# Optimization experiments

Measured on AMD Instinct MI355X. Metric: run time of the kernel, lower is better.

The kernel has to match this reference:

```python
import jax, jax.numpy as jnp
import numpy as np

N_NODES = 100000

def setup_inputs() -> dict:
    key = jax.random.key(0)
    k1, k2, k3, k4 = jax.random.split(key, 4)
    nfeat, nhid = 128, 128
    features = jax.random.normal(k1, (N_NODES, nfeat), dtype=jnp.float32)
    edges = jax.random.randint(k2, (2, 1600000), 0, N_NODES, dtype=jnp.int64)
    # Linear(nfeature, nhidden) params (PyTorch layout: W [out, in], b [out])
    bound = 1.0 / np.sqrt(nfeat)
    W = jax.random.uniform(k3, (nhid, nfeat), dtype=jnp.float32, minval=-bound, maxval=bound)
    b = jax.random.uniform(k4, (nhid,), dtype=jnp.float32, minval=-bound, maxval=bound)
    return {"features": features, "edges": edges, "W": W, "b": b}

def reference(features, edges, W, b):
    n = features.shape[0]
    # add self loops
    loops = jnp.arange(n, dtype=edges.dtype)
    row = jnp.concatenate([edges[0], loops])  # source
    col = jnp.concatenate([edges[1], loops])  # target
    # linear transform
    x = features @ W.T + b  # [N, nhid]
    # degree over source indices (PyG message uses degree(row, size[0]))
    deg = jax.ops.segment_sum(jnp.ones_like(row, dtype=x.dtype), row, num_segments=n)
    dis = jax.lax.rsqrt(deg)  # deg >= 1 thanks to self loops
    norm = dis[row] * dis[col]  # [E']
    msgs = norm[:, None] * x[row]  # gather + scale, [E', nhid]
    out = jax.ops.segment_sum(msgs, col, num_segments=n)  # scatter-add to targets
    return out
```

## Files before the change

kernel.cpp:

```cpp
#include <hip/hip_runtime.h>

#define NFEAT 128
#define CH 25600
#define CH2 (CH / 2)

typedef __attribute__((ext_vector_type(8))) short bf16x8;
typedef __attribute__((ext_vector_type(4))) float f32x4;

static __device__ __forceinline__ short f2bf(float f) {
    unsigned u = __builtin_bit_cast(unsigned, f);
    unsigned r = (u + 0x7fff + ((u >> 16) & 1)) >> 16;
    return (short)r;
}
static __device__ __forceinline__ float bf2f(short s) {
    unsigned u = ((unsigned)(unsigned short)s) << 16;
    return __builtin_bit_cast(float, u);
}

__launch_bounds__(256)
__global__ void hist16_kernel(const int* __restrict__ rows, const int* __restrict__ cols,
                              unsigned int* __restrict__ ph_row, unsigned int* __restrict__ ph_col,
                              int* __restrict__ rank, int E, int n, int W, int log_epb) {
    __shared__ unsigned int h[CH2];
    const int b = blockIdx.x;
    const int c0 = blockIdx.y * CH;
    const int z = blockIdx.z;
    const int* __restrict__ keys = z ? cols : rows;
    unsigned int* __restrict__ ph = z ? ph_col : ph_row;

    for (int i = threadIdx.x; i < CH2; i += 256) h[i] = 0;
    __syncthreads();

    const int lo = b << log_epb;
    const int hi = min(E, lo + (1 << log_epb));
    const int t = threadIdx.x;

    int full = (hi - lo) >> 10;
    for (int it = 0; it < full; ++it) {
        int e0 = lo + (it << 10) + t * 4;
        int4 kk = *(const int4*)(keys + e0);
        int k0 = kk.x - c0, k1 = kk.y - c0, k2 = kk.z - c0, k3 = kk.w - c0;
        if ((unsigned)k0 < CH) {
            unsigned old = atomicAdd(&h[k0 >> 1], 1u << ((k0 & 1) * 16));
            if (z) rank[e0 + 0] = (old >> ((k0 & 1) * 16)) & 0xffff;
        }
        if ((unsigned)k1 < CH) {
            unsigned old = atomicAdd(&h[k1 >> 1], 1u << ((k1 & 1) * 16));
            if (z) rank[e0 + 1] = (old >> ((k1 & 1) * 16)) & 0xffff;
        }
        if ((unsigned)k2 < CH) {
            unsigned old = atomicAdd(&h[k2 >> 1], 1u << ((k2 & 1) * 16));
            if (z) rank[e0 + 2] = (old >> ((k2 & 1) * 16)) & 0xffff;
        }
        if ((unsigned)k3 < CH) {
            unsigned old = atomicAdd(&h[k3 >> 1], 1u << ((k3 & 1) * 16));
            if (z) rank[e0 + 3] = (old >> ((k3 & 1) * 16)) & 0xffff;
        }
    }
    for (int e = lo + (full << 10) + t; e < hi; e += 256) {
        int k = keys[e] - c0;
        if ((unsigned)k < CH) {
            unsigned old = atomicAdd(&h[k >> 1], 1u << ((k & 1) * 16));
            if (z) rank[e] = (old >> ((k & 1) * 16)) & 0xffff;
        }
    }
    __syncthreads();

    int wbase = c0 >> 1;
    for (int i = threadIdx.x; i < CH2; i += 256) {
        int w = wbase + i;
        if (w < W) ph[(size_t)b * W + w] = h[i];
    }
}

__global__ void cum_kernel(const unsigned short* __restrict__ ph_row,
                           unsigned short* __restrict__ ph_col,
                           float* __restrict__ dis, int* __restrict__ colcnt, int NB, int n) {
    int k = blockIdx.x * 256 + threadIdx.x;
    if (k >= n) return;
    int rs = 0;
    for (int b = 0; b < NB; ++b) rs += ph_row[(size_t)b * n + k];
    dis[k] = rsqrtf(1.0f + (float)rs);
    int acc = 0;
    for (int b = 0; b < NB; ++b) {
        int v = ph_col[(size_t)b * n + k];
        ph_col[(size_t)b * n + k] = (unsigned short)acc;
        acc += v;
    }
    colcnt[k] = acc;
}

__global__ void scan_bsum_kernel(const int* __restrict__ cnt, int* __restrict__ bsum, int n) {
    __shared__ int s[256];
    int base = blockIdx.x * 1024;
    int t = threadIdx.x;
    int v = 0;
#pragma unroll
    for (int i = 0; i < 4; ++i) {
        int idx = base + t * 4 + i;
        if (idx < n) v += cnt[idx];
    }
    s[t] = v;
    __syncthreads();
    for (int o = 128; o > 0; o >>= 1) {
        if (t < o) s[t] += s[t + o];
        __syncthreads();
    }
    if (t == 0) bsum[blockIdx.x] = s[0];
}

__global__ void scan_top_kernel(int* __restrict__ bsum, int nb) {
    __shared__ int s[256];
    int t = threadIdx.x;
    int v = (t < nb) ? bsum[t] : 0;
    s[t] = v;
    __syncthreads();
    for (int o = 1; o < 256; o <<= 1) {
        int add = (t >= o) ? s[t - o] : 0;
        __syncthreads();
        s[t] += add;
        __syncthreads();
    }
    if (t < nb) bsum[t] = s[t] - v;
}

__global__ void scan_write_kernel(const int* __restrict__ cnt, const int* __restrict__ bsum,
                                  int* __restrict__ off, int n) {
    __shared__ int s[256];
    int base = blockIdx.x * 1024;
    int t = threadIdx.x;
    int v[4];
    int sum = 0;
#pragma unroll
    for (int i = 0; i < 4; ++i) {
        int idx = base + t * 4 + i;
        v[i] = (idx < n) ? cnt[idx] : 0;
        sum += v[i];
    }
    s[t] = sum;
    __syncthreads();
    for (int o = 1; o < 256; o <<= 1) {
        int add = (t >= o) ? s[t - o] : 0;
        __syncthreads();
        s[t] += add;
        __syncthreads();
    }
    int p = bsum[blockIdx.x] + s[t] - sum;
#pragma unroll
    for (int i = 0; i < 4; ++i) {
        int idx = base + t * 4 + i;
        if (idx < n) { off[idx] = p; p += v[i]; }
    }
}

__global__ void scatter2_kernel(const int* __restrict__ rows, const int* __restrict__ cols,
                                const int* __restrict__ rank, const unsigned short* __restrict__ ph_col,
                                const int* __restrict__ off, int* __restrict__ rows_buf,
                                int E, int n, int log_epb) {
    int base = blockIdx.x * 1024 + threadIdx.x;
#pragma unroll
    for (int u = 0; u < 4; ++u) {
        int e = base + u * 256;
        if (e < E) {
            int k = cols[e];
            int b = e >> log_epb;
            int pos = off[k] + (int)ph_col[(size_t)b * n + k] + rank[e];
            rows_buf[pos] = rows[e];
        }
    }
}

__launch_bounds__(256, 2)
__global__ void gemm_mfma_kernel(const float* __restrict__ feat, const float* __restrict__ W,
                                 const float* __restrict__ b, float* __restrict__ x, int n) {
    __shared__ short whi[16384];
    __shared__ short wlo[16384];

    const int t = threadIdx.x;

    {
        int c = t >> 1;
        int kbase = (t & 1) * 64;
        int ct = c >> 4;
        int cl = c & 15;
#pragma unroll
        for (int kc = 0; kc < 8; ++kc) {
            int k0 = kbase + kc * 8;
            const float4* src = (const float4*)(W + (size_t)c * NFEAT + k0);
            float4 fa = src[0];
            float4 fb = src[1];
            float fv[8] = {fa.x, fa.y, fa.z, fa.w, fb.x, fb.y, fb.z, fb.w};
            short h8[8], l8[8];
#pragma unroll
            for (int i = 0; i < 8; ++i) {
                short hi = f2bf(fv[i]);
                h8[i] = hi;
                l8[i] = f2bf(fv[i] - bf2f(hi));
            }
            int kq = k0 >> 5;
            int lane = ((k0 & 31) >> 3) * 16 + cl;
            int idx = ((ct * 4 + kq) * 64 + lane) * 8;
            *(bf16x8*)&whi[idx] = *(bf16x8*)h8;
            *(bf16x8*)&wlo[idx] = *(bf16x8*)l8;
        }
    }
    __syncthreads();

    const int lane = t & 63;
    const int w = t >> 6;
    const int r0 = blockIdx.x * 64 + w * 16;
    const int arow = r0 + (lane & 15);
    const int koff = (lane >> 4) * 8;

    bf16x8 ahi[4], alo[4];
#pragma unroll
    for (int kq = 0; kq < 4; ++kq) {
        float fv[8] = {0, 0, 0, 0, 0, 0, 0, 0};
        if (arow < n) {
            const float4* src = (const float4*)(feat + (size_t)arow * NFEAT + kq * 32 + koff);
            float4 fa = src[0];
            float4 fb = src[1];
            fv[0] = fa.x; fv[1] = fa.y; fv[2] = fa.z; fv[3] = fa.w;
            fv[4] = fb.x; fv[5] = fb.y; fv[6] = fb.z; fv[7] = fb.w;
        }
        short h8[8], l8[8];
#pragma unroll
        for (int i = 0; i < 8; ++i) {
            short hi = f2bf(fv[i]);
            h8[i] = hi;
            l8[i] = f2bf(fv[i] - bf2f(hi));
        }
        ahi[kq] = *(bf16x8*)h8;
        alo[kq] = *(bf16x8*)l8;
    }

#pragma unroll
    for (int ct = 0; ct < 8; ++ct) {
        f32x4 acc = {0.f, 0.f, 0.f, 0.f};
#pragma unroll
        for (int kq = 0; kq < 4; ++kq) {
            int idx = ((ct * 4 + kq) * 64 + lane) * 8;
            bf16x8 bh = *(const bf16x8*)&whi[idx];
            bf16x8 bl = *(const bf16x8*)&wlo[idx];
            acc = __builtin_amdgcn_mfma_f32_16x16x32_bf16(ahi[kq], bh, acc, 0, 0, 0);
            acc = __builtin_amdgcn_mfma_f32_16x16x32_bf16(alo[kq], bh, acc, 0, 0, 0);
            acc = __builtin_amdgcn_mfma_f32_16x16x32_bf16(ahi[kq], bl, acc, 0, 0, 0);
        }
        int col = ct * 16 + (lane & 15);
        float bb = b[col];
#pragma unroll
        for (int reg = 0; reg < 4; ++reg) {
            int row = r0 + (lane >> 4) * 4 + reg;
            if (row < n) x[(size_t)row * NFEAT + col] = acc[reg] + bb;
        }
    }
}

__launch_bounds__(256)
__global__ void gather_kernel(const int* __restrict__ rows_buf, const int* __restrict__ off,
                              const int* __restrict__ cnt, const float* __restrict__ x,
                              const float* __restrict__ dis, float* __restrict__ out, int n) {
    int lane = threadIdx.x & 63;
    int h = lane >> 5;
    int fl = lane & 31;
    int c = blockIdx.x * 4 + (threadIdx.x >> 6);
    if (c >= n) return;

    float disc = dis[c];
    int start = off[c];
    int len = cnt[c];
    const float4* x4 = (const float4*)x;

    float4 acc = make_float4(0.f, 0.f, 0.f, 0.f);
    if (h == 0) {
        float4 xv = x4[(size_t)c * 32 + fl];
        float sl = disc * disc;
        acc.x = xv.x * sl; acc.y = xv.y * sl; acc.z = xv.z * sl; acc.w = xv.w * sl;
    }

    for (int base = 0; base < len; base += 64) {
        int m = min(64, len - base);
        int r_l = 0;
        float nrm_l = 0.0f;
        if (lane < m) {
            r_l = rows_buf[start + base + lane];
            nrm_l = dis[r_l] * disc;
        }
        int pairs = (m + 1) >> 1;
#pragma unroll 4
        for (int jj = 0; jj < pairs; ++jj) {
            int src = 2 * jj + h;
            int r = __shfl(r_l, src);
            float nm = __shfl(nrm_l, src);
            float4 a = x4[(size_t)r * 32 + fl];
            acc.x = fmaf(a.x, nm, acc.x);
            acc.y = fmaf(a.y, nm, acc.y);
            acc.z = fmaf(a.z, nm, acc.z);
            acc.w = fmaf(a.w, nm, acc.w);
        }
    }

    acc.x += __shfl_xor(acc.x, 32);
    acc.y += __shfl_xor(acc.y, 32);
    acc.z += __shfl_xor(acc.z, 32);
    acc.w += __shfl_xor(acc.w, 32);

    if (h == 0) ((float4*)out)[(size_t)c * 32 + fl] = acc;
}

extern "C" void kernel_launch(void* const* d_in, const int* in_sizes, int n_in,
                              void* d_out, int out_size, void* d_ws, size_t ws_size,
                              hipStream_t stream) {
    const float* feat = (const float*)d_in[0];
    const int*   edges = (const int*)d_in[1];
    const float* W = (const float*)d_in[2];
    const float* b = (const float*)d_in[3];
    float* out = (float*)d_out;

    int n = in_sizes[0] / NFEAT;
    int E = in_sizes[1] / 2;
    const int* row = edges;
    const int* col = edges + E;

    int Wd = (n + 1) / 2;
    int nchunk = (n + CH - 1) / CH;

    size_t fixed = (size_t)n * NFEAT + 3 * (size_t)n + 2 * (size_t)E + 256;
    int log_epb = 16;
    int NB = (E + (1 << 16) - 1) >> 16;
    for (int lg = 14; lg <= 16; ++lg) {
        int nb_try = (E + (1 << lg) - 1) >> lg;
        size_t words = fixed + 2 * (size_t)nb_try * Wd;
        if (words * 4 <= ws_size) { log_epb = lg; NB = nb_try; break; }
    }

    float* x        = (float*)d_ws;
    float* dis      = x + (size_t)n * NFEAT;
    int*   colcnt   = (int*)(dis + n);
    int*   off      = colcnt + n;
    int*   rows_buf = off + n;
    int*   rank     = rows_buf + E;
    int*   bsum     = rank + E;
    unsigned int* ph_row = (unsigned int*)(bsum + 256);
    unsigned int* ph_col = ph_row + (size_t)NB * Wd;

    int nb = (n + 1023) / 1024;

    dim3 hgrid(NB, nchunk, 2);
    hist16_kernel<<<hgrid, 256, 0, stream>>>(row, col, ph_row, ph_col, rank, E, n, Wd, log_epb);

    cum_kernel<<<(n + 255) / 256, 256, 0, stream>>>((const unsigned short*)ph_row,
                                                    (unsigned short*)ph_col, dis, colcnt, NB, n);

    scan_bsum_kernel<<<nb, 256, 0, stream>>>(colcnt, bsum, n);
    scan_top_kernel<<<1, 256, 0, stream>>>(bsum, nb);
    scan_write_kernel<<<nb, 256, 0, stream>>>(colcnt, bsum, off, n);

    scatter2_kernel<<<(E + 1023) / 1024, 256, 0, stream>>>(row, col, rank,
                                                           (const unsigned short*)ph_col,
                                                           off, rows_buf, E, n, log_epb);

    gemm_mfma_kernel<<<(n + 63) / 64, 256, 0, stream>>>(feat, W, b, x, n);

    gather_kernel<<<(n + 3) / 4, 256, 0, stream>>>(rows_buf, off, colcnt, x, dis, out, n);
}
```

Measured before the change: 395.2 us.

## Store transformed features as bf16 and gather with quarter-wave rows

The GEMM drops the split-bf16 (hi/lo) three-MFMA emulation of fp32 and uses a single bf16 MFMA, then writes x as bf16 instead of fp32. This halves the intermediate buffer and the bytes moved in the gather. The gather kernel now lets each 16-lane quarter of a wave read one 256-byte bf16 row, so four edges are processed per step, and the partial sums are reduced across quarters with shuffles. Accuracy drops to plain bf16 for both the GEMM inputs and the stored activations, which may exceed the tolerance.

```diff
diff --git a/kernel.cpp b/kernel.cpp
--- a/kernel.cpp
+++ b/kernel.cpp
@@ -12,9 +12,11 @@
     unsigned r = (u + 0x7fff + ((u >> 16) & 1)) >> 16;
     return (short)r;
 }
-static __device__ __forceinline__ float bf2f(short s) {
-    unsigned u = ((unsigned)(unsigned short)s) << 16;
-    return __builtin_bit_cast(float, u);
+static __device__ __forceinline__ float bflo(unsigned u) {
+    return __builtin_bit_cast(float, u << 16);
+}
+static __device__ __forceinline__ float bfhi(unsigned u) {
+    return __builtin_bit_cast(float, u & 0xffff0000u);
 }
 
 __launch_bounds__(256)
@@ -170,11 +172,10 @@
     }
 }
 
-__launch_bounds__(256, 2)
-__global__ void gemm_mfma_kernel(const float* __restrict__ feat, const float* __restrict__ W,
-                                 const float* __restrict__ b, float* __restrict__ x, int n) {
-    __shared__ short whi[16384];
-    __shared__ short wlo[16384];
+__launch_bounds__(256)
+__global__ void gemm_bf16_kernel(const float* __restrict__ feat, const float* __restrict__ W,
+                                 const float* __restrict__ b, unsigned short* __restrict__ x16, int n) {
+    __shared__ short wb[16384];
 
     const int t = threadIdx.x;
 
@@ -190,18 +191,13 @@
             float4 fa = src[0];
             float4 fb = src[1];
             float fv[8] = {fa.x, fa.y, fa.z, fa.w, fb.x, fb.y, fb.z, fb.w};
-            short h8[8], l8[8];
-#pragma unroll
-            for (int i = 0; i < 8; ++i) {
-                short hi = f2bf(fv[i]);
-                h8[i] = hi;
-                l8[i] = f2bf(fv[i] - bf2f(hi));
-            }
+            short h8[8];
+#pragma unroll
+            for (int i = 0; i < 8; ++i) h8[i] = f2bf(fv[i]);
             int kq = k0 >> 5;
             int lane = ((k0 & 31) >> 3) * 16 + cl;
             int idx = ((ct * 4 + kq) * 64 + lane) * 8;
-            *(bf16x8*)&whi[idx] = *(bf16x8*)h8;
-            *(bf16x8*)&wlo[idx] = *(bf16x8*)l8;
+            *(bf16x8*)&wb[idx] = *(bf16x8*)h8;
         }
     }
     __syncthreads();
@@ -212,7 +208,7 @@
     const int arow = r0 + (lane & 15);
     const int koff = (lane >> 4) * 8;
 
-    bf16x8 ahi[4], alo[4];
+    bf16x8 a[4];
 #pragma unroll
     for (int kq = 0; kq < 4; ++kq) {
         float fv[8] = {0, 0, 0, 0, 0, 0, 0, 0};
@@ -223,15 +219,10 @@
             fv[0] = fa.x; fv[1] = fa.y; fv[2] = fa.z; fv[3] = fa.w;
             fv[4] = fb.x; fv[5] = fb.y; fv[6] = fb.z; fv[7] = fb.w;
         }
-        short h8[8], l8[8];
-#pragma unroll
-        for (int i = 0; i < 8; ++i) {
-            short hi = f2bf(fv[i]);
-            h8[i] = hi;
-            l8[i] = f2bf(fv[i] - bf2f(hi));
-        }
-        ahi[kq] = *(bf16x8*)h8;
-        alo[kq] = *(bf16x8*)l8;
+        short h8[8];
+#pragma unroll
+        for (int i = 0; i < 8; ++i) h8[i] = f2bf(fv[i]);
+        a[kq] = *(bf16x8*)h8;
     }
 
 #pragma unroll
@@ -240,43 +231,35 @@
 #pragma unroll
         for (int kq = 0; kq < 4; ++kq) {
             int idx = ((ct * 4 + kq) * 64 + lane) * 8;
-            bf16x8 bh = *(const bf16x8*)&whi[idx];
-            bf16x8 bl = *(const bf16x8*)&wlo[idx];
-            acc = __builtin_amdgcn_mfma_f32_16x16x32_bf16(ahi[kq], bh, acc, 0, 0, 0);
-            acc = __builtin_amdgcn_mfma_f32_16x16x32_bf16(alo[kq], bh, acc, 0, 0, 0);
-            acc = __builtin_amdgcn_mfma_f32_16x16x32_bf16(ahi[kq], bl, acc, 0, 0, 0);
+            bf16x8 bh = *(const bf16x8*)&wb[idx];
+            acc = __builtin_amdgcn_mfma_f32_16x16x32_bf16(a[kq], bh, acc, 0, 0, 0);
         }
         int col = ct * 16 + (lane & 15);
         float bb = b[col];
 #pragma unroll
         for (int reg = 0; reg < 4; ++reg) {
             int row = r0 + (lane >> 4) * 4 + reg;
-            if (row < n) x[(size_t)row * NFEAT + col] = acc[reg] + bb;
+            if (row < n) x16[(size_t)row * NFEAT + col] = (unsigned short)f2bf(acc[reg] + bb);
         }
     }
 }
 
 __launch_bounds__(256)
 __global__ void gather_kernel(const int* __restrict__ rows_buf, const int* __restrict__ off,
-                              const int* __restrict__ cnt, const float* __restrict__ x,
+                              const int* __restrict__ cnt, const unsigned short* __restrict__ x16,
                               const float* __restrict__ dis, float* __restrict__ out, int n) {
     int lane = threadIdx.x & 63;
-    int h = lane >> 5;
-    int fl = lane & 31;
+    int q = lane >> 4;
+    int fq = lane & 15;
     int c = blockIdx.x * 4 + (threadIdx.x >> 6);
     if (c >= n) return;
 
     float disc = dis[c];
     int start = off[c];
     int len = cnt[c];
-    const float4* x4 = (const float4*)x;
-
-    float4 acc = make_float4(0.f, 0.f, 0.f, 0.f);
-    if (h == 0) {
-        float4 xv = x4[(size_t)c * 32 + fl];
-        float sl = disc * disc;
-        acc.x = xv.x * sl; acc.y = xv.y * sl; acc.z = xv.z * sl; acc.w = xv.w * sl;
-    }
+    const uint4* xv = (const uint4*)x16;
+
+    float a0 = 0.f, a1 = 0.f, a2 = 0.f, a3 = 0.f, a4 = 0.f, a5 = 0.f, a6 = 0.f, a7 = 0.f;
 
     for (int base = 0; base < len; base += 64) {
         int m = min(64, len - base);
@@ -286,26 +269,42 @@
             r_l = rows_buf[start + base + lane];
             nrm_l = dis[r_l] * disc;
         }
-        int pairs = (m + 1) >> 1;
+        int quads = (m + 3) >> 2;
 #pragma unroll 4
-        for (int jj = 0; jj < pairs; ++jj) {
-            int src = 2 * jj + h;
+        for (int jj = 0; jj < quads; ++jj) {
+            int src = 4 * jj + q;
             int r = __shfl(r_l, src);
             float nm = __shfl(nrm_l, src);
-            float4 a = x4[(size_t)r * 32 + fl];
-            acc.x = fmaf(a.x, nm, acc.x);
-            acc.y = fmaf(a.y, nm, acc.y);
-            acc.z = fmaf(a.z, nm, acc.z);
-            acc.w = fmaf(a.w, nm, acc.w);
-        }
-    }
-
-    acc.x += __shfl_xor(acc.x, 32);
-    acc.y += __shfl_xor(acc.y, 32);
-    acc.z += __shfl_xor(acc.z, 32);
-    acc.w += __shfl_xor(acc.w, 32);
-
-    if (h == 0) ((float4*)out)[(size_t)c * 32 + fl] = acc;
+            if (src < m) {
+                uint4 v = xv[(size_t)r * 16 + fq];
+                a0 = fmaf(bflo(v.x), nm, a0); a1 = fmaf(bfhi(v.x), nm, a1);
+                a2 = fmaf(bflo(v.y), nm, a2); a3 = fmaf(bfhi(v.y), nm, a3);
+                a4 = fmaf(bflo(v.z), nm, a4); a5 = fmaf(bfhi(v.z), nm, a5);
+                a6 = fmaf(bflo(v.w), nm, a6); a7 = fmaf(bfhi(v.w), nm, a7);
+            }
+        }
+    }
+
+    a0 += __shfl_xor(a0, 16); a1 += __shfl_xor(a1, 16);
+    a2 += __shfl_xor(a2, 16); a3 += __shfl_xor(a3, 16);
+    a4 += __shfl_xor(a4, 16); a5 += __shfl_xor(a5, 16);
+    a6 += __shfl_xor(a6, 16); a7 += __shfl_xor(a7, 16);
+    a0 += __shfl_xor(a0, 32); a1 += __shfl_xor(a1, 32);
+    a2 += __shfl_xor(a2, 32); a3 += __shfl_xor(a3, 32);
+    a4 += __shfl_xor(a4, 32); a5 += __shfl_xor(a5, 32);
+    a6 += __shfl_xor(a6, 32); a7 += __shfl_xor(a7, 32);
+
+    if (q == 0) {
+        float sl = disc * disc;
+        uint4 v = xv[(size_t)c * 16 + fq];
+        a0 = fmaf(bflo(v.x), sl, a0); a1 = fmaf(bfhi(v.x), sl, a1);
+        a2 = fmaf(bflo(v.y), sl, a2); a3 = fmaf(bfhi(v.y), sl, a3);
+        a4 = fmaf(bflo(v.z), sl, a4); a5 = fmaf(bfhi(v.z), sl, a5);
+        a6 = fmaf(bflo(v.w), sl, a6); a7 = fmaf(bfhi(v.w), sl, a7);
+        float4* o = (float4*)(out + (size_t)c * NFEAT + fq * 8);
+        o[0] = make_float4(a0, a1, a2, a3);
+        o[1] = make_float4(a4, a5, a6, a7);
+    }
 }
 
 extern "C" void kernel_launch(void* const* d_in, const int* in_sizes, int n_in,
@@ -325,7 +324,7 @@
     int Wd = (n + 1) / 2;
     int nchunk = (n + CH - 1) / CH;
 
-    size_t fixed = (size_t)n * NFEAT + 3 * (size_t)n + 2 * (size_t)E + 256;
+    size_t fixed = (size_t)n * 64 + 3 * (size_t)n + 2 * (size_t)E + 256;
     int log_epb = 16;
     int NB = (E + (1 << 16) - 1) >> 16;
     for (int lg = 14; lg <= 16; ++lg) {
@@ -334,8 +333,8 @@
         if (words * 4 <= ws_size) { log_epb = lg; NB = nb_try; break; }
     }
 
-    float* x        = (float*)d_ws;
-    float* dis      = x + (size_t)n * NFEAT;
+    unsigned short* x16 = (unsigned short*)d_ws;
+    float* dis      = (float*)(x16 + (size_t)n * NFEAT);
     int*   colcnt   = (int*)(dis + n);
     int*   off      = colcnt + n;
     int*   rows_buf = off + n;
@@ -360,7 +359,7 @@
                                                            (const unsigned short*)ph_col,
                                                            off, rows_buf, E, n, log_epb);
 
-    gemm_mfma_kernel<<<(n + 63) / 64, 256, 0, stream>>>(feat, W, b, x, n);
-
-    gather_kernel<<<(n + 3) / 4, 256, 0, stream>>>(rows_buf, off, colcnt, x, dis, out, n);
-}
+    gemm_bf16_kernel<<<(n + 63) / 64, 256, 0, stream>>>(feat, W, b, x16, n);
+
+    gather_kernel<<<(n + 3) / 4, 256, 0, stream>>>(rows_buf, off, colcnt, x16, dis, out, n);
+}
```

New measurement: 335.3 us. 1.18x faster.
